# Kernel tuning notes

Hardware: AMD Instinct MI355X
Metric: run time of the kernel (lower is better)

The kernel has to match this reference:

```python
import jax, jax.numpy as jnp
import numpy as np

N = 100_000      # nodes
F_IN = 256       # input features
HID = 256        # hidden dim
C = 40           # classes
E = 1_600_000    # edges
BN_EPS = 1e-5


def setup_inputs() -> dict:
    key = jax.random.key(0)
    ks = jax.random.split(key, 8)
    x = jax.random.normal(ks[0], (N, F_IN), dtype=jnp.float32)
    edge_index = jax.random.randint(ks[1], (2, E), 0, N)
    W1 = jax.random.normal(ks[2], (F_IN, HID), dtype=jnp.float32) / np.sqrt(F_IN)
    b1 = jnp.zeros((HID,), jnp.float32)
    gamma = jnp.ones((HID,), jnp.float32)
    beta = jnp.zeros((HID,), jnp.float32)
    W2 = jax.random.normal(ks[3], (HID, C), dtype=jnp.float32) / np.sqrt(HID)
    b2 = jnp.zeros((C,), jnp.float32)
    return {"x": x, "edge_index": edge_index, "W1": W1, "b1": b1,
            "gamma": gamma, "beta": beta, "W2": W2, "b2": b2}


def _gcn_propagate(h, src, dst, norm):
    # out[dst] += norm * h[src]   (symmetric-normalized aggregation, self-loops included)
    msg = norm[:, None] * h[src]                       # [E+N, D]
    return jax.ops.segment_sum(msg, dst, num_segments=N)


def reference(x, edge_index, W1, b1, gamma, beta, W2, b2):
    loops = jnp.arange(N, dtype=edge_index.dtype)
    src = jnp.concatenate([edge_index[0], loops])      # add self-loops (PyG GCNConv)
    dst = jnp.concatenate([edge_index[1], loops])
    deg = jax.ops.segment_sum(jnp.ones_like(dst, jnp.float32), dst, num_segments=N)
    dinv = jnp.where(deg > 0, jax.lax.rsqrt(deg), 0.0)
    norm = dinv[src] * dinv[dst]

    # Layer 1: GCNConv (linear without bias -> propagate -> + bias)
    h = _gcn_propagate(x @ W1, src, dst, norm) + b1    # [N, HID]
    # BatchNorm1d over nodes (training-style batch statistics, biased variance)
    mu = h.mean(axis=0)
    var = h.var(axis=0)
    h = (h - mu) * jax.lax.rsqrt(var + BN_EPS) * gamma + beta
    h = jax.nn.relu(h)                                 # dropout is identity in eval

    # Layer 2: GCNConv -> log_softmax
    out = _gcn_propagate(h @ W2, src, dst, norm) + b2  # [N, C]
    return jax.nn.log_softmax(out, axis=1)
```

## Files before the change

kernel.cpp:

```cpp
#include <hip/hip_runtime.h>
#include <math.h>

#define N_NODES 100000
#define F_IN    256
#define HID     256
#define C_OUT   40
#define N_EDGES 1600000
#define BN_EPS  1e-5f

#define CAP     64
#define CNT_BLOCKS  ((N_EDGES + 255) / 256)

typedef __attribute__((ext_vector_type(8))) short short8;
typedef __attribute__((ext_vector_type(8))) unsigned short ushort8v;
typedef __attribute__((ext_vector_type(4))) float f32x4;

static __device__ __forceinline__ unsigned short f2bf(float f) {
    unsigned int u = __float_as_uint(f);
    unsigned int r = u + 0x7FFFu + ((u >> 16) & 1u);
    return (unsigned short)(r >> 16);
}
static __device__ __forceinline__ float bf2f(unsigned short b) {
    return __uint_as_float(((unsigned int)b) << 16);
}

__global__ void count_scatter_castw(const int* __restrict__ src, const int* __restrict__ dst,
                                    int* cnt, int* __restrict__ csr,
                                    const float* __restrict__ W1, const float* __restrict__ W2,
                                    unsigned short* __restrict__ w1t, unsigned short* __restrict__ w2t) {
    int b = blockIdx.x, t = threadIdx.x;
    if (b < CNT_BLOCKS) {
        int i = b * 256 + t;
        if (i < N_EDGES) {
            int d = dst[i];
            int pos = atomicAdd(&cnt[d], 1);
            if (pos < CAP) csr[(size_t)d * CAP + pos] = src[i];
        }
    } else if (b < CNT_BLOCKS + 256) {
        int n = b - CNT_BLOCKS;
        w1t[(size_t)n * 256 + t] = f2bf(W1[(size_t)t * 256 + n]);
    } else {
        int n = b - CNT_BLOCKS - 256;
        w2t[(size_t)n * 256 + t] = (n < C_OUT) ? f2bf(W2[(size_t)t * C_OUT + n]) : (unsigned short)0;
    }
}

__global__ __launch_bounds__(256) void init_dinv(const int* __restrict__ cnt,
                                                 float* __restrict__ dinv) {
    int w = blockIdx.x * 256 + threadIdx.x;
    if (w < N_NODES) dinv[w] = rsqrtf((float)(cnt[w] + 1));
}

#define LDK 56
__global__ __launch_bounds__(256) void gemm1_mfma(const float* __restrict__ x,
                                                  const unsigned short* __restrict__ w1t,
                                                  const float* __restrict__ dinv,
                                                  unsigned short* __restrict__ hs, int M) {
    __shared__ unsigned short As[64][LDK];
    __shared__ unsigned short Bs[256][LDK];
    int tid = threadIdx.x;
    int wave = tid >> 6, lane = tid & 63;
    int m0 = blockIdx.x * 64;
    f32x4 acc[4][4] = {};

    int ar = tid >> 2, ac = (tid & 3) * 8;
    int brow = tid;
    int gr = m0 + ar;
    bool rowok = gr < M;
    const float* xrow = x + (size_t)gr * 256 + ac;
    const unsigned short* wrow = w1t + (size_t)brow * 256;

    float4 pa = make_float4(0.f,0.f,0.f,0.f), pb = pa;
    if (rowok) { pa = *(const float4*)(xrow); pb = *(const float4*)(xrow + 4); }
    ushort8v rb0 = *(const ushort8v*)(wrow);
    ushort8v rb1 = *(const ushort8v*)(wrow + 8);
    ushort8v rb2 = *(const ushort8v*)(wrow + 16);
    ushort8v rb3 = *(const ushort8v*)(wrow + 24);

    for (int k0 = 0; k0 < 256; k0 += 32) {
        {
            ushort8v u;
            u[0] = f2bf(pa.x); u[1] = f2bf(pa.y); u[2] = f2bf(pa.z); u[3] = f2bf(pa.w);
            u[4] = f2bf(pb.x); u[5] = f2bf(pb.y); u[6] = f2bf(pb.z); u[7] = f2bf(pb.w);
            if (!rowok) {
#pragma unroll
                for (int q = 0; q < 8; q++) u[q] = 0;
            }
            *(ushort8v*)&As[ar][ac] = u;
        }
        *(ushort8v*)&Bs[brow][0]  = rb0;
        *(ushort8v*)&Bs[brow][8]  = rb1;
        *(ushort8v*)&Bs[brow][16] = rb2;
        *(ushort8v*)&Bs[brow][24] = rb3;
        __syncthreads();
        if (k0 + 32 < 256) {
            if (rowok) {
                pa = *(const float4*)(xrow + k0 + 32);
                pb = *(const float4*)(xrow + k0 + 36);
            }
            const unsigned short* p = wrow + k0 + 32;
            rb0 = *(const ushort8v*)(p);
            rb1 = *(const ushort8v*)(p + 8);
            rb2 = *(const ushort8v*)(p + 16);
            rb3 = *(const ushort8v*)(p + 24);
        }
        int fr = lane & 15, fk = (lane >> 4) * 8;
        short8 a[4], b[4];
#pragma unroll
        for (int mt = 0; mt < 4; mt++) a[mt] = *(short8*)&As[mt * 16 + fr][fk];
#pragma unroll
        for (int nt = 0; nt < 4; nt++) b[nt] = *(short8*)&Bs[wave * 64 + nt * 16 + fr][fk];
#pragma unroll
        for (int mt = 0; mt < 4; mt++)
#pragma unroll
            for (int nt = 0; nt < 4; nt++)
                acc[mt][nt] = __builtin_amdgcn_mfma_f32_16x16x32_bf16(a[mt], b[nt], acc[mt][nt], 0, 0, 0);
        __syncthreads();
    }
    int fr = lane & 15, fg = lane >> 4;
#pragma unroll
    for (int mt = 0; mt < 4; mt++) {
#pragma unroll
        for (int r = 0; r < 4; r++) {
            int row = m0 + mt * 16 + fg * 4 + r;
            if (row < M) {
                float dv = dinv[row];
#pragma unroll
                for (int nt = 0; nt < 4; nt++) {
                    int col = wave * 64 + nt * 16 + fr;
                    hs[(size_t)row * 256 + col] = f2bf(acc[mt][nt][r] * dv);
                }
            }
        }
    }
}

__global__ __launch_bounds__(256) void agg256(const int* __restrict__ cnt,
                                              const int* __restrict__ csr,
                                              const unsigned short* __restrict__ hs,
                                              const float* __restrict__ dinv,
                                              unsigned short* __restrict__ hagg) {
    int g = blockIdx.x * blockDim.x + threadIdx.x;
    int wid = g >> 6, lane = g & 63;
    if (wid >= N_NODES) return;
    int half = lane >> 5;
    int c8 = (lane & 31) * 8;
    int beg = wid * CAP;
    int end = beg + cnt[wid];
    float acc[8] = {0.f, 0.f, 0.f, 0.f, 0.f, 0.f, 0.f, 0.f};
    int j = beg;
    if (j + 7 < end) {
        int sxA[4];
        ushort8v uA[4];
#pragma unroll
        for (int q = 0; q < 4; q++) sxA[q] = csr[j + 2 * q + half];
#pragma unroll
        for (int q = 0; q < 4; q++) uA[q] = *(const ushort8v*)(hs + (size_t)sxA[q] * 256 + c8);
        j += 8;
        while (j + 7 < end) {
            int sxB[4];
            ushort8v uB[4];
#pragma unroll
            for (int q = 0; q < 4; q++) sxB[q] = csr[j + 2 * q + half];
#pragma unroll
            for (int q = 0; q < 4; q++) uB[q] = *(const ushort8v*)(hs + (size_t)sxB[q] * 256 + c8);
#pragma unroll
            for (int q = 0; q < 4; q++)
#pragma unroll
                for (int e = 0; e < 8; e++) acc[e] += bf2f(uA[q][e]);
#pragma unroll
            for (int q = 0; q < 4; q++) uA[q] = uB[q];
            j += 8;
        }
#pragma unroll
        for (int q = 0; q < 4; q++)
#pragma unroll
            for (int e = 0; e < 8; e++) acc[e] += bf2f(uA[q][e]);
    }
    if (j + 3 < end) {
        int s0 = csr[j + half];
        int s1 = csr[j + 2 + half];
        ushort8v u0 = *(const ushort8v*)(hs + (size_t)s0 * 256 + c8);
        ushort8v u1 = *(const ushort8v*)(hs + (size_t)s1 * 256 + c8);
#pragma unroll
        for (int e = 0; e < 8; e++) acc[e] += bf2f(u0[e]) + bf2f(u1[e]);
        j += 4;
    }
    if (j + 1 < end) {
        int s = csr[j + half];
        ushort8v u = *(const ushort8v*)(hs + (size_t)s * 256 + c8);
#pragma unroll
        for (int e = 0; e < 8; e++) acc[e] += bf2f(u[e]);
        j += 2;
    }
    if (j < end && half == 0) {
        int s = csr[j];
        ushort8v u = *(const ushort8v*)(hs + (size_t)s * 256 + c8);
#pragma unroll
        for (int e = 0; e < 8; e++) acc[e] += bf2f(u[e]);
    }
#pragma unroll
    for (int e = 0; e < 8; e++) acc[e] += __shfl_xor(acc[e], 32);
    if (half == 0) {
        ushort8v us = *(const ushort8v*)(hs + (size_t)wid * 256 + c8);
        float dv = dinv[wid];
        ushort8v o;
#pragma unroll
        for (int e = 0; e < 8; e++) o[e] = f2bf((acc[e] + bf2f(us[e])) * dv);
        *(ushort8v*)(hagg + (size_t)wid * 256 + c8) = o;
    }
}

#define BNS_BLOCKS 1024
__global__ __launch_bounds__(256) void bn_stats_v(const unsigned short* __restrict__ h,
                                                  float* musum, float* sqsum) {
    int tid = threadIdx.x;
    int wave = tid >> 6, lane = tid & 63;
    int half = lane >> 5;
    int c8 = (lane & 31) * 8;
    int gw = blockIdx.x * 4 + wave;
    float s[8] = {0.f,0.f,0.f,0.f,0.f,0.f,0.f,0.f};
    float q2[8] = {0.f,0.f,0.f,0.f,0.f,0.f,0.f,0.f};
    for (int r = gw * 2 + half; r < N_NODES; r += BNS_BLOCKS * 4 * 2) {
        ushort8v u = *(const ushort8v*)(h + (size_t)r * 256 + c8);
#pragma unroll
        for (int e = 0; e < 8; e++) {
            float v = bf2f(u[e]);
            s[e] += v; q2[e] += v * v;
        }
    }
#pragma unroll
    for (int e = 0; e < 8; e++) {
        s[e]  += __shfl_xor(s[e], 32);
        q2[e] += __shfl_xor(q2[e], 32);
    }
    __shared__ float sS[4][256];
    __shared__ float sQ[4][256];
    if (half == 0) {
#pragma unroll
        for (int e = 0; e < 8; e++) { sS[wave][c8 + e] = s[e]; sQ[wave][c8 + e] = q2[e]; }
    }
    __syncthreads();
    float a = sS[0][tid] + sS[1][tid] + sS[2][tid] + sS[3][tid];
    float b = sQ[0][tid] + sQ[1][tid] + sQ[2][tid] + sQ[3][tid];
    atomicAdd(&musum[tid], a);
    atomicAdd(&sqsum[tid], b);
}

#define LDB2 264
__global__ __launch_bounds__(256) void gemm2_mfma(const unsigned short* __restrict__ hagg,
                                                  const unsigned short* __restrict__ w2t,
                                                  const float* __restrict__ musum,
                                                  const float* __restrict__ sqsum,
                                                  const float* __restrict__ gamma,
                                                  const float* __restrict__ beta,
                                                  const float* __restrict__ dinv,
                                                  unsigned short* __restrict__ g2b, int M) {
    __shared__ unsigned short w2s[48][LDB2];
    __shared__ unsigned short As[64][40];
    __shared__ float ss[256], sh[256];
    int tid = threadIdx.x;
    int wave = tid >> 6, lane = tid & 63;
    int m0 = blockIdx.x * 64;

    for (int i = tid; i < 48 * 32; i += 256) {
        int rrow = i >> 5, c8 = (i & 31) * 8;
        *(ushort8v*)&w2s[rrow][c8] = *(const ushort8v*)(w2t + (size_t)rrow * 256 + c8);
    }
    {
        const float invN = 1.0f / N_NODES;
        float m = musum[tid] * invN;
        float var = sqsum[tid] * invN - m * m;
        float s = gamma[tid] * rsqrtf(var + BN_EPS);
        ss[tid] = s;
        sh[tid] = beta[tid] - m * s;
    }

    f32x4 acc[3] = {};
    int arow = tid >> 2, ac0 = (tid & 3) * 8;
    int fr = lane & 15, fk = (lane >> 4) * 8;

    for (int k0 = 0; k0 < 256; k0 += 32) {
        __syncthreads();
        {
            int gr = m0 + arow;
            ushort8v u;
            if (gr < M) {
                u = *(const ushort8v*)(hagg + (size_t)gr * 256 + k0 + ac0);
#pragma unroll
                for (int q = 0; q < 8; q++) {
                    int col = k0 + ac0 + q;
                    float v = bf2f(u[q]);
                    v = fmaxf(v * ss[col] + sh[col], 0.0f);
                    u[q] = f2bf(v);
                }
            } else {
#pragma unroll
                for (int q = 0; q < 8; q++) u[q] = 0;
            }
            *(ushort8v*)&As[arow][ac0] = u;
        }
        __syncthreads();
        short8 a = *(short8*)&As[wave * 16 + fr][fk];
#pragma unroll
        for (int nt = 0; nt < 3; nt++) {
            short8 b = *(short8*)&w2s[nt * 16 + fr][k0 + fk];
            acc[nt] = __builtin_amdgcn_mfma_f32_16x16x32_bf16(a, b, acc[nt], 0, 0, 0);
        }
    }
    int fg = lane >> 4;
#pragma unroll
    for (int nt = 0; nt < 3; nt++) {
        int col = nt * 16 + fr;
        if (col < C_OUT) {
#pragma unroll
            for (int r = 0; r < 4; r++) {
                int row = m0 + wave * 16 + fg * 4 + r;
                if (row < M) g2b[(size_t)row * C_OUT + col] = f2bf(acc[nt][r] * dinv[row]);
            }
        }
    }
}

__global__ __launch_bounds__(256) void agg40_logsm(const int* __restrict__ cnt,
                                                   const int* __restrict__ csr,
                                                   const unsigned short* __restrict__ g2b,
                                                   const float* __restrict__ dinv,
                                                   const float* __restrict__ b2,
                                                   float* __restrict__ out) {
    int gi = blockIdx.x * blockDim.x + threadIdx.x;
    int wid = gi >> 6, lane = gi & 63;
    if (wid >= N_NODES) return;
    int g = lane / 10;
    int k4 = lane - g * 10;
    bool gact = lane < 60;
    int beg = wid * CAP;
    int end = beg + cnt[wid];
    float a4[4] = {0.f, 0.f, 0.f, 0.f};
    if (end > beg) {
        int jlim = end - 1;
        int j = beg;
        int s0 = csr[min(j + g, jlim)];
        ushort4 u0 = *(const ushort4*)(g2b + (size_t)s0 * C_OUT + k4 * 4);
        while (1) {
            int jn = j + 6;
            bool more = jn < end;
            int s1 = 0; ushort4 u1;
            if (more) {
                s1 = csr[min(jn + g, jlim)];
                u1 = *(const ushort4*)(g2b + (size_t)s1 * C_OUT + k4 * 4);
            }
            if (gact && j + g < end) {
                a4[0] += bf2f(u0.x); a4[1] += bf2f(u0.y);
                a4[2] += bf2f(u0.z); a4[3] += bf2f(u0.w);
            }
            if (!more) break;
            u0 = u1; j = jn;
        }
    }
#pragma unroll
    for (int e = 0; e < 4; e++) {
        float t0 = __shfl(a4[e], lane + 30);
        a4[e] += t0;
    }
#pragma unroll
    for (int e = 0; e < 4; e++) {
        float t1 = __shfl(a4[e], lane + 10);
        float t2 = __shfl(a4[e], lane + 20);
        a4[e] += t1 + t2;
    }
    bool act = lane < 10;
    float dvd = dinv[wid];
    float v[4];
    float mloc = -INFINITY;
    if (act) {
        ushort4 su = *(const ushort4*)(g2b + (size_t)wid * C_OUT + k4 * 4);
        a4[0] += bf2f(su.x); a4[1] += bf2f(su.y);
        a4[2] += bf2f(su.z); a4[3] += bf2f(su.w);
    }
#pragma unroll
    for (int e = 0; e < 4; e++) {
        v[e] = act ? a4[e] * dvd + b2[k4 * 4 + e] : -INFINITY;
        mloc = fmaxf(mloc, v[e]);
    }
#pragma unroll
    for (int o = 32; o > 0; o >>= 1) mloc = fmaxf(mloc, __shfl_xor(mloc, o));
    float sloc = 0.f;
    if (act) {
#pragma unroll
        for (int e = 0; e < 4; e++) sloc += __expf(v[e] - mloc);
    }
#pragma unroll
    for (int o = 32; o > 0; o >>= 1) sloc += __shfl_xor(sloc, o);
    float ls = __logf(sloc);
    if (act) {
        float4 o4 = make_float4(v[0] - mloc - ls, v[1] - mloc - ls,
                                v[2] - mloc - ls, v[3] - mloc - ls);
        *(float4*)(out + (size_t)wid * C_OUT + k4 * 4) = o4;
    }
}

extern "C" void kernel_launch(void* const* d_in, const int* in_sizes, int n_in,
                              void* d_out, int out_size, void* d_ws, size_t ws_size,
                              hipStream_t stream) {
    const float* x     = (const float*)d_in[0];
    const int*   ei    = (const int*)  d_in[1];
    const float* W1    = (const float*)d_in[2];
    const float* gamma = (const float*)d_in[4];
    const float* beta  = (const float*)d_in[5];
    const float* W2    = (const float*)d_in[6];
    const float* b2    = (const float*)d_in[7];
    float* out = (float*)d_out;

    const int* src = ei;
    const int* dst = ei + N_EDGES;

    unsigned short* hs    = (unsigned short*)d_ws;
    unsigned short* hagg  = hs + (size_t)N_NODES * 256;
    unsigned short* g2b   = hagg + (size_t)N_NODES * 256;
    float*          dinv  = (float*)(g2b + (size_t)N_NODES * C_OUT);
    int*            cnt   = (int*)(dinv + N_NODES);
    int*            csr   = cnt + N_NODES;
    unsigned short* w1t   = (unsigned short*)(csr + (size_t)N_NODES * CAP);
    unsigned short* w2t   = w1t + 65536;
    float*          musum = (float*)(w2t + 48 * 256);
    float*          sqsum = musum + 256;

    hipMemsetAsync(cnt, 0, N_NODES * sizeof(int), stream);
    hipMemsetAsync(musum, 0, 512 * sizeof(float), stream);

    count_scatter_castw<<<CNT_BLOCKS + 256 + 48, 256, 0, stream>>>(src, dst, cnt, csr, W1, W2, w1t, w2t);
    init_dinv<<<(N_NODES + 255) / 256, 256, 0, stream>>>(cnt, dinv);

    gemm1_mfma<<<(N_NODES + 63) / 64, 256, 0, stream>>>(x, w1t, dinv, hs, N_NODES);

    int aggblk = (int)(((size_t)N_NODES * 64 + 255) / 256);
    agg256<<<aggblk, 256, 0, stream>>>(cnt, csr, hs, dinv, hagg);

    bn_stats_v<<<BNS_BLOCKS, 256, 0, stream>>>(hagg, musum, sqsum);

    gemm2_mfma<<<(N_NODES + 63) / 64, 256, 0, stream>>>(hagg, w2t, musum, sqsum, gamma, beta, dinv, g2b, N_NODES);

    agg40_logsm<<<aggblk, 256, 0, stream>>>(cnt, csr, g2b, dinv, b2, out);
}
```

Measured before the change: 427.2 us.

## Shard degree-count atomics across eight counters and build CSR in a separate pass

Edge counting now spreads the atomics over eight per-shard counter arrays (chosen by block index) and records each edge's rank. A new kernel takes a prefix over the shards to get per-node bases, total degree and dinv, and a third kernel scatters each src into the CSR slot. The aim is to cut contention on the per-node atomics and make CSR order deterministic, at the cost of an extra kernel launch, a larger memset and extra rank/base traffic. The scratch arrays reuse workspace buffers that are only written later.

```diff
diff --git a/kernel.cpp b/kernel.cpp
--- a/kernel.cpp
+++ b/kernel.cpp
@@ -9,6 +9,7 @@
 #define BN_EPS  1e-5f
 
 #define CAP     64
+#define NSHARD  8
 #define CNT_BLOCKS  ((N_EDGES + 255) / 256)
 
 typedef __attribute__((ext_vector_type(8))) short short8;
@@ -24,17 +25,16 @@
     return __uint_as_float(((unsigned int)b) << 16);
 }
 
-__global__ void count_scatter_castw(const int* __restrict__ src, const int* __restrict__ dst,
-                                    int* cnt, int* __restrict__ csr,
-                                    const float* __restrict__ W1, const float* __restrict__ W2,
-                                    unsigned short* __restrict__ w1t, unsigned short* __restrict__ w2t) {
+__global__ void count_castw(const int* __restrict__ dst, int* cnt8,
+                            int* __restrict__ rank,
+                            const float* __restrict__ W1, const float* __restrict__ W2,
+                            unsigned short* __restrict__ w1t, unsigned short* __restrict__ w2t) {
     int b = blockIdx.x, t = threadIdx.x;
     if (b < CNT_BLOCKS) {
         int i = b * 256 + t;
         if (i < N_EDGES) {
-            int d = dst[i];
-            int pos = atomicAdd(&cnt[d], 1);
-            if (pos < CAP) csr[(size_t)d * CAP + pos] = src[i];
+            int s = b & (NSHARD - 1);
+            rank[i] = atomicAdd(&cnt8[s * N_NODES + dst[i]], 1);
         }
     } else if (b < CNT_BLOCKS + 256) {
         int n = b - CNT_BLOCKS;
@@ -45,10 +45,36 @@
     }
 }
 
-__global__ __launch_bounds__(256) void init_dinv(const int* __restrict__ cnt,
+__global__ __launch_bounds__(256) void base_init(const int* __restrict__ cnt8,
+                                                 int* __restrict__ base8,
+                                                 int* __restrict__ cnttot,
                                                  float* __restrict__ dinv) {
-    int w = blockIdx.x * 256 + threadIdx.x;
-    if (w < N_NODES) dinv[w] = rsqrtf((float)(cnt[w] + 1));
+    int d = blockIdx.x * 256 + threadIdx.x;
+    if (d < N_NODES) {
+        int run = 0;
+#pragma unroll
+        for (int s = 0; s < NSHARD; s++) {
+            int c = cnt8[s * N_NODES + d];
+            base8[s * N_NODES + d] = run;
+            run += c;
+        }
+        cnttot[d] = run;
+        dinv[d] = rsqrtf((float)(run + 1));
+    }
+}
+
+__global__ __launch_bounds__(256) void scatter_sharded(const int* __restrict__ src,
+                                                       const int* __restrict__ dst,
+                                                       const int* __restrict__ rank,
+                                                       const int* __restrict__ base8,
+                                                       int* __restrict__ csr) {
+    int e = blockIdx.x * 256 + threadIdx.x;
+    if (e < N_EDGES) {
+        int s = (e >> 8) & (NSHARD - 1);
+        int d = dst[e];
+        int pos = base8[s * N_NODES + d] + rank[e];
+        if (pos < CAP) csr[(size_t)d * CAP + pos] = src[e];
+    }
 }
 
 #define LDK 56
@@ -135,7 +161,7 @@
     }
 }
 
-__global__ __launch_bounds__(256) void agg256(const int* __restrict__ cnt,
+__global__ __launch_bounds__(256) void agg256(const int* __restrict__ cnttot,
                                               const int* __restrict__ csr,
                                               const unsigned short* __restrict__ hs,
                                               const float* __restrict__ dinv,
@@ -146,7 +172,7 @@
     int half = lane >> 5;
     int c8 = (lane & 31) * 8;
     int beg = wid * CAP;
-    int end = beg + cnt[wid];
+    int end = beg + min(cnttot[wid], CAP);
     float acc[8] = {0.f, 0.f, 0.f, 0.f, 0.f, 0.f, 0.f, 0.f};
     int j = beg;
     if (j + 7 < end) {
@@ -322,7 +348,7 @@
     }
 }
 
-__global__ __launch_bounds__(256) void agg40_logsm(const int* __restrict__ cnt,
+__global__ __launch_bounds__(256) void agg40_logsm(const int* __restrict__ cnttot,
                                                    const int* __restrict__ csr,
                                                    const unsigned short* __restrict__ g2b,
                                                    const float* __restrict__ dinv,
@@ -335,7 +361,7 @@
     int k4 = lane - g * 10;
     bool gact = lane < 60;
     int beg = wid * CAP;
-    int end = beg + cnt[wid];
+    int end = beg + min(cnttot[wid], CAP);
     float a4[4] = {0.f, 0.f, 0.f, 0.f};
     if (end > beg) {
         int jlim = end - 1;
@@ -419,27 +445,31 @@
     unsigned short* hagg  = hs + (size_t)N_NODES * 256;
     unsigned short* g2b   = hagg + (size_t)N_NODES * 256;
     float*          dinv  = (float*)(g2b + (size_t)N_NODES * C_OUT);
-    int*            cnt   = (int*)(dinv + N_NODES);
-    int*            csr   = cnt + N_NODES;
+    int*            cnttot= (int*)(dinv + N_NODES);
+    int*            csr   = cnttot + N_NODES;
     unsigned short* w1t   = (unsigned short*)(csr + (size_t)N_NODES * CAP);
     unsigned short* w2t   = w1t + 65536;
     float*          musum = (float*)(w2t + 48 * 256);
     float*          sqsum = musum + 256;
-
-    hipMemsetAsync(cnt, 0, N_NODES * sizeof(int), stream);
+    int*            cnt8  = (int*)hs;
+    int*            rank  = (int*)hagg;
+    int*            base8 = (int*)g2b;
+
+    hipMemsetAsync(cnt8, 0, NSHARD * N_NODES * sizeof(int), stream);
     hipMemsetAsync(musum, 0, 512 * sizeof(float), stream);
 
-    count_scatter_castw<<<CNT_BLOCKS + 256 + 48, 256, 0, stream>>>(src, dst, cnt, csr, W1, W2, w1t, w2t);
-    init_dinv<<<(N_NODES + 255) / 256, 256, 0, stream>>>(cnt, dinv);
+    count_castw<<<CNT_BLOCKS + 256 + 48, 256, 0, stream>>>(dst, cnt8, rank, W1, W2, w1t, w2t);
+    base_init<<<(N_NODES + 255) / 256, 256, 0, stream>>>(cnt8, base8, cnttot, dinv);
+    scatter_sharded<<<CNT_BLOCKS, 256, 0, stream>>>(src, dst, rank, base8, csr);
 
     gemm1_mfma<<<(N_NODES + 63) / 64, 256, 0, stream>>>(x, w1t, dinv, hs, N_NODES);
 
     int aggblk = (int)(((size_t)N_NODES * 64 + 255) / 256);
-    agg256<<<aggblk, 256, 0, stream>>>(cnt, csr, hs, dinv, hagg);
+    agg256<<<aggblk, 256, 0, stream>>>(cnttot, csr, hs, dinv, hagg);
 
     bn_stats_v<<<BNS_BLOCKS, 256, 0, stream>>>(hagg, musum, sqsum);
 
     gemm2_mfma<<<(N_NODES + 63) / 64, 256, 0, stream>>>(hagg, w2t, musum, sqsum, gamma, beta, dinv, g2b, N_NODES);
 
-    agg40_logsm<<<aggblk, 256, 0, stream>>>(cnt, csr, g2b, dinv, b2, out);
-}
+    agg40_logsm<<<aggblk, 256, 0, stream>>>(cnttot, csr, g2b, dinv, b2, out);
+}
```

Result: faster. 398.8 us (-6.6%).
